# Kernel tuning notes

Hardware: AMD Instinct MI355X
Metric: run time of the kernel (lower is better)

Reference implementation:

```python
import jax, jax.numpy as jnp
import numpy as np

H, I, E, K = 1024, 2816, 8, 2  # hidden, intermediate, n_experts, topk
B, S = 2, 2048


def setup_inputs() -> dict:
    key = jax.random.key(0)
    ks = jax.random.split(key, 6)
    def init(k, shape, fan_in):
        return (jax.random.normal(k, shape, jnp.float32) / np.sqrt(fan_in)).astype(jnp.float32)
    return {
        "x": jax.random.normal(ks[0], (B, S, H), jnp.float32),
        "Wgate": init(ks[1], (H, E), H),   # gating Linear weight (in,out layout)
        "bgate": jnp.zeros((E,), jnp.float32),  # gating Linear bias (nn.Linear default bias=True)
        "Wg": init(ks[2], (E, H, I), H),   # stacked gate_proj, mlp_bias=False
        "Wu": init(ks[3], (E, H, I), H),   # stacked up_proj
        "Wd": init(ks[4], (E, I, H), I),   # stacked down_proj
    }


def reference(x, Wgate, bgate, Wg, Wu, Wd):
    Bb, Ss, Hd = x.shape
    xf = x.reshape(-1, Hd)                       # [N, H] flattened tokens
    logits = xf @ Wgate + bgate                  # [N, E] gate logits
    topv, topi = jax.lax.top_k(logits, K)        # [N, K]
    N = xf.shape[0]
    # sparse combine weights: raw top-k LOGITS (no softmax), zeros elsewhere
    # (faithful to torch: scatter of logits_topk into -inf mask; -inf slots
    #  are never read since only selected experts contribute)
    combine = jnp.zeros_like(logits).at[jnp.arange(N)[:, None], topi].set(topv)  # [N, E]
    # dense grouped SwiGLU over all experts, then sparse combine
    g = jnp.einsum('nh,ehi->nei', xf, Wg)        # [N, E, I]
    u = jnp.einsum('nh,ehi->nei', xf, Wu)        # [N, E, I]
    h = jax.nn.silu(g) * u                       # [N, E, I]
    eo = jnp.einsum('nei,eih->neh', h, Wd)       # [N, E, H]
    out = jnp.einsum('neh,ne->nh', eo, combine).reshape(Bb, Ss, Hd)
    return out, logits
```

## Files before the change

### kernel.cpp

```cpp
#include <hip/hip_runtime.h>

#define HDIM 1024
#define IDIM 2816
#define NEXP 8
#define NTOK 4096
#define NROWS 8192
#define RPAD 8320
#define MAXT 71
#define GU_NYT 44
#define DN_NYT 8
#define GU_NWG (MAXT * GU_NYT)
#define DN_NWG (MAXT * DN_NYT)

typedef short bf16x8 __attribute__((ext_vector_type(8)));
typedef float f32x4 __attribute__((ext_vector_type(4)));
typedef unsigned short u16x8 __attribute__((ext_vector_type(8)));

static __device__ __forceinline__ unsigned short f2bf(float f) {
    union { float f; unsigned int i; } v; v.f = f;
    return (unsigned short)((v.i + 0x7fffu + ((v.i >> 16) & 1u)) >> 16);
}

static __device__ __forceinline__ void gload16(const void* g, void* l) {
    __builtin_amdgcn_global_load_lds(
        (const __attribute__((address_space(1))) unsigned int*)g,
        (__attribute__((address_space(3))) unsigned int*)l, 16, 0, 0);
}

__global__ __launch_bounds__(256) void gating_kernel(
    const float* __restrict__ x, const float* __restrict__ Wgate,
    const float* __restrict__ bgate, float* __restrict__ logits_out,
    int* __restrict__ counts, int* __restrict__ topi, float* __restrict__ topv)
{
    int wave = (blockIdx.x << 2) + (threadIdx.x >> 6);
    int lane = threadIdx.x & 63;
    if (wave >= NTOK) return;
    const float* xr = x + (size_t)wave * HDIM;

    double acc[NEXP];
#pragma unroll
    for (int e = 0; e < NEXP; ++e) acc[e] = 0.0;

    for (int it = 0; it < HDIM / 64; ++it) {
        int h = lane + (it << 6);
        float xv = xr[h];
        const float* wr = Wgate + (size_t)h * NEXP;
#pragma unroll
        for (int e = 0; e < NEXP; ++e) acc[e] += (double)xv * (double)wr[e];
    }
#pragma unroll
    for (int e = 0; e < NEXP; ++e) {
        double v = acc[e];
        for (int off = 32; off; off >>= 1) v += __shfl_xor(v, off, 64);
        acc[e] = v + (double)bgate[e];
    }
    float lf[NEXP];
#pragma unroll
    for (int e = 0; e < NEXP; ++e) lf[e] = (float)acc[e];

    if (lane < NEXP) logits_out[(size_t)wave * NEXP + lane] = lf[lane];

    if (lane == 0) {
        int i1 = 0; float v1 = lf[0];
#pragma unroll
        for (int e = 1; e < NEXP; ++e) if (lf[e] > v1) { v1 = lf[e]; i1 = e; }
        int i2 = -1; float v2 = -3.0e38f;
#pragma unroll
        for (int e = 0; e < NEXP; ++e) {
            if (e == i1) continue;
            if (lf[e] > v2) { v2 = lf[e]; i2 = e; }
        }
        topi[wave * 2 + 0] = i1; topv[wave * 2 + 0] = v1;
        topi[wave * 2 + 1] = i2; topv[wave * 2 + 1] = v2;
        atomicAdd(&counts[i1], 1);
        atomicAdd(&counts[i2], 1);
    }
}

__global__ void offsets_kernel(const int* __restrict__ counts,
                               int* __restrict__ offs, int* __restrict__ cursor,
                               int* __restrict__ ntile, int* __restrict__ te,
                               int* __restrict__ tm0)
{
    if (threadIdx.x == 0 && blockIdx.x == 0) {
        int s = 0;
        for (int e = 0; e < NEXP; ++e) { offs[e] = s; cursor[e] = s; s += counts[e]; }
        offs[NEXP] = s;
        int nt = 0;
        for (int e = 0; e < NEXP; ++e) {
            int c = counts[e], base = offs[e];
            for (int mt = 0; mt * 128 < c; ++mt) { te[nt] = e; tm0[nt] = base + mt * 128; ++nt; }
        }
        *ntile = nt;
    }
}

__global__ __launch_bounds__(256) void scatter_kernel(
    const float* __restrict__ x, const int* __restrict__ topi,
    const float* __restrict__ topv, int* __restrict__ cursor,
    float* __restrict__ row_w, int* __restrict__ tok_of,
    unsigned short* __restrict__ Xg)
{
    int p = (blockIdx.x << 2) + (threadIdx.x >> 6);
    int lane = threadIdx.x & 63;
    if (p >= NROWS) return;
    int n = p >> 1;
    int e = topi[p];
    float w = topv[p];
    int pos = 0;
    if (lane == 0) {
        pos = atomicAdd(&cursor[e], 1);
        row_w[pos] = w;
        tok_of[pos] = n;
    }
    pos = __shfl(pos, 0, 64);
    const float* xr = x + (size_t)n * HDIM;
    unsigned short* dst = Xg + (size_t)pos * HDIM;
#pragma unroll
    for (int it = 0; it < HDIM / 256; ++it) {
        int idx = (it * 64 + lane) * 4;
        float4 v = *reinterpret_cast<const float4*>(&xr[idx]);
        ushort4 o;
        o.x = f2bf(v.x); o.y = f2bf(v.y); o.z = f2bf(v.z); o.w = f2bf(v.w);
        *reinterpret_cast<ushort4*>(&dst[idx]) = o;
    }
}

__global__ __launch_bounds__(256) void transpose_cvt_gu_kernel(
    const float* __restrict__ Wg, const float* __restrict__ Wu,
    unsigned short* __restrict__ W2)
{
    __shared__ unsigned short lds[64 * 66];
    const int kind = blockIdx.z;
    const int e = blockIdx.y;
    const float* s0 = (kind ? Wu : Wg) + (size_t)e * HDIM * IDIM;
    unsigned short* d0 = W2 + (size_t)e * 2 * IDIM * HDIM;
    const int TC = IDIM / 64;
    int tt = blockIdx.x;
    int tr = tt / TC, tc = tt % TC;
    int tid = threadIdx.x;
    {
        int r = tid >> 2, c0 = (tid & 3) << 4;
        const float* s = s0 + (size_t)(tr * 64 + r) * IDIM + tc * 64 + c0;
        float4 v0 = *reinterpret_cast<const float4*>(s);
        float4 v1 = *reinterpret_cast<const float4*>(s + 4);
        float4 v2 = *reinterpret_cast<const float4*>(s + 8);
        float4 v3 = *reinterpret_cast<const float4*>(s + 12);
        unsigned short* lr_ = &lds[r * 66 + c0];
        lr_[0]  = f2bf(v0.x); lr_[1]  = f2bf(v0.y); lr_[2]  = f2bf(v0.z); lr_[3]  = f2bf(v0.w);
        lr_[4]  = f2bf(v1.x); lr_[5]  = f2bf(v1.y); lr_[6]  = f2bf(v1.z); lr_[7]  = f2bf(v1.w);
        lr_[8]  = f2bf(v2.x); lr_[9]  = f2bf(v2.y); lr_[10] = f2bf(v2.z); lr_[11] = f2bf(v2.w);
        lr_[12] = f2bf(v3.x); lr_[13] = f2bf(v3.y); lr_[14] = f2bf(v3.z); lr_[15] = f2bf(v3.w);
    }
    __syncthreads();
    {
        int c = tid >> 2, q0 = (tid & 3) << 4;
        u16x8 o0, o1;
#pragma unroll
        for (int j = 0; j < 8; ++j) o0[j] = lds[(q0 + j) * 66 + c];
#pragma unroll
        for (int j = 0; j < 8; ++j) o1[j] = lds[(q0 + 8 + j) * 66 + c];
        int i = tc * 64 + c;
        int r2 = ((i >> 4) << 5) + (kind << 4) + (i & 15);
        unsigned short* d = d0 + (size_t)r2 * HDIM + tr * 64 + q0;
        *reinterpret_cast<u16x8*>(d) = o0;
        *reinterpret_cast<u16x8*>(d + 8) = o1;
    }
}

__global__ __launch_bounds__(256) void transpose_cvt_d_kernel(
    const float* __restrict__ Wd, unsigned short* __restrict__ Wdt)
{
    __shared__ unsigned short lds[64 * 66];
    const int e = blockIdx.y;
    const float* s0 = Wd + (size_t)e * IDIM * HDIM;
    unsigned short* d0 = Wdt + (size_t)e * HDIM * IDIM;
    const int TC = HDIM / 64;
    int tt = blockIdx.x;
    int tr = tt / TC, tc = tt % TC;
    int tid = threadIdx.x;
    {
        int r = tid >> 2, c0 = (tid & 3) << 4;
        const float* s = s0 + (size_t)(tr * 64 + r) * HDIM + tc * 64 + c0;
        float4 v0 = *reinterpret_cast<const float4*>(s);
        float4 v1 = *reinterpret_cast<const float4*>(s + 4);
        float4 v2 = *reinterpret_cast<const float4*>(s + 8);
        float4 v3 = *reinterpret_cast<const float4*>(s + 12);
        unsigned short* lr_ = &lds[r * 66 + c0];
        lr_[0]  = f2bf(v0.x); lr_[1]  = f2bf(v0.y); lr_[2]  = f2bf(v0.z); lr_[3]  = f2bf(v0.w);
        lr_[4]  = f2bf(v1.x); lr_[5]  = f2bf(v1.y); lr_[6]  = f2bf(v1.z); lr_[7]  = f2bf(v1.w);
        lr_[8]  = f2bf(v2.x); lr_[9]  = f2bf(v2.y); lr_[10] = f2bf(v2.z); lr_[11] = f2bf(v2.w);
        lr_[12] = f2bf(v3.x); lr_[13] = f2bf(v3.y); lr_[14] = f2bf(v3.z); lr_[15] = f2bf(v3.w);
    }
    __syncthreads();
    {
        int c = tid >> 2, q0 = (tid & 3) << 4;
        u16x8 o0, o1;
#pragma unroll
        for (int j = 0; j < 8; ++j) o0[j] = lds[(q0 + j) * 66 + c];
#pragma unroll
        for (int j = 0; j < 8; ++j) o1[j] = lds[(q0 + 8 + j) * 66 + c];
        unsigned short* d = d0 + (size_t)(tc * 64 + c) * IDIM + tr * 64 + q0;
        *reinterpret_cast<u16x8*>(d) = o0;
        *reinterpret_cast<u16x8*>(d + 8) = o1;
    }
}

__global__ __launch_bounds__(256, 4) void gateup_kernel(
    const unsigned short* __restrict__ Xg,
    const unsigned short* __restrict__ W2,
    const int* __restrict__ offs,
    const int* __restrict__ ntile, const int* __restrict__ te,
    const int* __restrict__ tm0, unsigned short* __restrict__ hbuf)
{
    __shared__ unsigned short As[128 * 64];
    __shared__ unsigned short Bs[128 * 64];

    int bid = blockIdx.x;
    int xcd = bid & 7, rest = bid >> 3;
    const int q = GU_NWG / 8, r = GU_NWG % 8;
    int wg = (xcd < r ? xcd * (q + 1) : r * (q + 1) + (xcd - r) * q) + rest;
    int t = wg % MAXT;
    int ny = wg / MAXT;

    if (t >= *ntile) return;
    const int e = te[t];
    const int m0 = tm0[t];
    const int r1 = offs[e + 1];
    const int n0 = ny * 128;

    const unsigned short* wb = W2 + (size_t)e * 2 * IDIM * HDIM;

    const int tid = threadIdx.x;
    const int lane = tid & 63, wv = tid >> 6;
    const int wr = (wv >> 1) * 64, wc = (wv & 1) * 64;
    const int lr = lane & 15, kg = (lane >> 4) * 8;
    const int srow = lane >> 3;
    const int scol = (lane & 7) * 8;

    f32x4 zero = {0.f, 0.f, 0.f, 0.f};
    f32x4 acc[4][4];
#pragma unroll
    for (int m = 0; m < 4; ++m)
#pragma unroll
        for (int n = 0; n < 4; ++n) acc[m][n] = zero;

    for (int k0 = 0; k0 < HDIM; k0 += 64) {
        __syncthreads();
#pragma unroll
        for (int i = 0; i < 4; ++i) {
            int chunk = i * 4 + wv;
            int row = chunk * 8 + srow;
            gload16(&Xg[(size_t)(m0 + row) * HDIM + k0 + scol], &As[chunk * 512 + lane * 8]);
            gload16(&wb[(size_t)(n0 + row) * HDIM + k0 + scol], &Bs[chunk * 512 + lane * 8]);
        }
        __syncthreads();

#pragma unroll
        for (int ks = 0; ks < 2; ++ks) {
            bf16x8 af[4], bf[4];
#pragma unroll
            for (int m = 0; m < 4; ++m)
                af[m] = *reinterpret_cast<const bf16x8*>(&As[(wr + m * 16 + lr) * 64 + ks * 32 + kg]);
#pragma unroll
            for (int n = 0; n < 4; ++n)
                bf[n] = *reinterpret_cast<const bf16x8*>(&Bs[(wc + n * 16 + lr) * 64 + ks * 32 + kg]);
#pragma unroll
            for (int m = 0; m < 4; ++m)
#pragma unroll
                for (int n = 0; n < 4; ++n)
                    acc[m][n] = __builtin_amdgcn_mfma_f32_16x16x32_bf16(af[m], bf[n], acc[m][n], 0, 0, 0);
        }
    }

    const int rr = (lane >> 4) * 4;
    const int iloc0 = ((wc >> 5) << 4) + lr;
    const int col0 = ny * 64 + iloc0;
#pragma unroll
    for (int m = 0; m < 4; ++m) {
#pragma unroll
        for (int j = 0; j < 4; ++j) {
            int grow = m0 + wr + m * 16 + rr + j;
            if (grow < r1) {
                unsigned short* hr = &hbuf[(size_t)grow * IDIM + col0];
                float g0 = acc[m][0][j], u0 = acc[m][1][j];
                float g1 = acc[m][2][j], u1 = acc[m][3][j];
                hr[0]  = f2bf(g0 / (1.0f + __expf(-g0)) * u0);
                hr[16] = f2bf(g1 / (1.0f + __expf(-g1)) * u1);
            }
        }
    }
}

__global__ __launch_bounds__(256, 4) void down_kernel(
    const unsigned short* __restrict__ hbuf,
    const unsigned short* __restrict__ Wdt,
    const int* __restrict__ offs,
    const int* __restrict__ ntile, const int* __restrict__ te,
    const int* __restrict__ tm0,
    const float* __restrict__ row_w, const int* __restrict__ tok_of,
    float* __restrict__ out)
{
    __shared__ unsigned short As[128 * 64];
    __shared__ unsigned short Bs[128 * 64];

    int bid = blockIdx.x;
    int xcd = bid & 7, rest = bid >> 3;
    int wg = xcd * (DN_NWG / 8) + rest;
    int t = wg % MAXT;
    int ny = wg / MAXT;

    if (t >= *ntile) return;
    const int e = te[t];
    const int m0 = tm0[t];
    const int r1 = offs[e + 1];
    const int n0 = ny * 128;

    const unsigned short* wd = Wdt + (size_t)e * HDIM * IDIM;

    const int tid = threadIdx.x;
    const int lane = tid & 63, wv = tid >> 6;
    const int wr = (wv >> 1) * 64, wc = (wv & 1) * 64;
    const int lr = lane & 15, kg = (lane >> 4) * 8;
    const int srow = lane >> 3;
    const int scol = (lane & 7) * 8;

    f32x4 zero = {0.f, 0.f, 0.f, 0.f};
    f32x4 acc[4][4];
#pragma unroll
    for (int m = 0; m < 4; ++m)
#pragma unroll
        for (int n = 0; n < 4; ++n) acc[m][n] = zero;

    for (int k0 = 0; k0 < IDIM; k0 += 64) {
        __syncthreads();
#pragma unroll
        for (int i = 0; i < 4; ++i) {
            int chunk = i * 4 + wv;
            int row = chunk * 8 + srow;
            gload16(&hbuf[(size_t)(m0 + row) * IDIM + k0 + scol], &As[chunk * 512 + lane * 8]);
            gload16(&wd[(size_t)(n0 + row) * IDIM + k0 + scol], &Bs[chunk * 512 + lane * 8]);
        }
        __syncthreads();

#pragma unroll
        for (int ks = 0; ks < 2; ++ks) {
            bf16x8 af[4], bf[4];
#pragma unroll
            for (int m = 0; m < 4; ++m)
                af[m] = *reinterpret_cast<const bf16x8*>(&As[(wr + m * 16 + lr) * 64 + ks * 32 + kg]);
#pragma unroll
            for (int n = 0; n < 4; ++n)
                bf[n] = *reinterpret_cast<const bf16x8*>(&Bs[(wc + n * 16 + lr) * 64 + ks * 32 + kg]);
#pragma unroll
            for (int m = 0; m < 4; ++m)
#pragma unroll
                for (int n = 0; n < 4; ++n)
                    acc[m][n] = __builtin_amdgcn_mfma_f32_16x16x32_bf16(af[m], bf[n], acc[m][n], 0, 0, 0);
        }
    }

    const int rr = (lane >> 4) * 4;
#pragma unroll
    for (int m = 0; m < 4; ++m) {
#pragma unroll
        for (int j = 0; j < 4; ++j) {
            int grow = m0 + wr + m * 16 + rr + j;
            if (grow < r1) {
                float w = row_w[grow];
                int tok = tok_of[grow];
                float* orow = out + (size_t)tok * HDIM + n0 + wc + lr;
#pragma unroll
                for (int n = 0; n < 4; ++n)
                    atomicAdd(&orow[n * 16], acc[m][n][j] * w);
            }
        }
    }
}

extern "C" void kernel_launch(void* const* d_in, const int* in_sizes, int n_in,
                              void* d_out, int out_size, void* d_ws, size_t ws_size,
                              hipStream_t stream)
{
    const float* x     = (const float*)d_in[0];
    const float* Wgate = (const float*)d_in[1];
    const float* bgate = (const float*)d_in[2];
    const float* Wg    = (const float*)d_in[3];
    const float* Wu    = (const float*)d_in[4];
    const float* Wd    = (const float*)d_in[5];
    float* out = (float*)d_out;
    float* logits = out + (size_t)NTOK * HDIM;

    char* ws = (char*)d_ws;
    unsigned short* Xg   = (unsigned short*)ws;
    unsigned short* hbuf = (unsigned short*)(ws + 17039360);
    unsigned short* W2   = (unsigned short*)(ws + 63897600);
    char* meta = ws + 156172288;
    int*   counts = (int*)(meta);
    int*   offs   = (int*)(meta + 64);
    int*   cursor = (int*)(meta + 128);
    int*   ntile  = (int*)(meta + 192);
    int*   te     = (int*)(meta + 256);
    int*   tm0    = (int*)(meta + 768);
    int*   topi   = (int*)(meta + 2048);
    float* topv   = (float*)(meta + 34816);
    float* row_w  = (float*)(meta + 67584);
    int*   tok_of = (int*)(meta + 100352);

    hipMemsetAsync(counts, 0, 32, stream);
    hipMemsetAsync(out, 0, (size_t)NTOK * HDIM * sizeof(float), stream);

    gating_kernel<<<NTOK / 4, 256, 0, stream>>>(x, Wgate, bgate, logits, counts, topi, topv);
    offsets_kernel<<<1, 64, 0, stream>>>(counts, offs, cursor, ntile, te, tm0);
    scatter_kernel<<<NROWS / 4, 256, 0, stream>>>(x, topi, topv, cursor, row_w, tok_of, Xg);

    transpose_cvt_gu_kernel<<<dim3((HDIM / 64) * (IDIM / 64), NEXP, 2), 256, 0, stream>>>(Wg, Wu, W2);

    gateup_kernel<<<GU_NWG, 256, 0, stream>>>(Xg, W2, offs, ntile, te, tm0, hbuf);

    transpose_cvt_d_kernel<<<dim3((IDIM / 64) * (HDIM / 64), NEXP), 256, 0, stream>>>(Wd, W2);

    down_kernel<<<DN_NWG, 256, 0, stream>>>(hbuf, W2, offs, ntile, te, tm0, row_w, tok_of, out);
}
```

Before: 515.2 us.

## Fuse weight transpose and bf16 conversion into grouped GEMM B-tile loads

Removes the two separate transpose/convert kernels for gate/up and down weights. The GEMM kernels now read fp32 weights directly, convert them to bf16 in registers and write them into LDS in a transposed, XOR-swizzled layout. The A loads are swizzled to match. The gate-up grid is regrouped so that 8 consecutive M-tiles share the same N-slice, for better weight reuse in L2. This avoids writing and rereading roughly 140MB of bf16 weights. In exchange, each tile reloads fp32 weights with scalar, non-async loads, and the conversion is now repeated in every workgroup that touches the same weight tile.

Measured after the change: 668.8 us. 1.3x slower.

```diff
diff --git a/kernel.cpp b/kernel.cpp
--- a/kernel.cpp
+++ b/kernel.cpp
@@ -9,12 +9,13 @@
 #define MAXT 71
 #define GU_NYT 44
 #define DN_NYT 8
-#define GU_NWG (MAXT * GU_NYT)
+#define GU_TG 8
+#define GU_NTG 9
+#define GU_NWG (GU_NTG * GU_NYT * GU_TG)
 #define DN_NWG (MAXT * DN_NYT)
 
 typedef short bf16x8 __attribute__((ext_vector_type(8)));
 typedef float f32x4 __attribute__((ext_vector_type(4)));
-typedef unsigned short u16x8 __attribute__((ext_vector_type(8)));
 
 static __device__ __forceinline__ unsigned short f2bf(float f) {
     union { float f; unsigned int i; } v; v.f = f;
@@ -126,89 +127,9 @@
     }
 }
 
-__global__ __launch_bounds__(256) void transpose_cvt_gu_kernel(
-    const float* __restrict__ Wg, const float* __restrict__ Wu,
-    unsigned short* __restrict__ W2)
-{
-    __shared__ unsigned short lds[64 * 66];
-    const int kind = blockIdx.z;
-    const int e = blockIdx.y;
-    const float* s0 = (kind ? Wu : Wg) + (size_t)e * HDIM * IDIM;
-    unsigned short* d0 = W2 + (size_t)e * 2 * IDIM * HDIM;
-    const int TC = IDIM / 64;
-    int tt = blockIdx.x;
-    int tr = tt / TC, tc = tt % TC;
-    int tid = threadIdx.x;
-    {
-        int r = tid >> 2, c0 = (tid & 3) << 4;
-        const float* s = s0 + (size_t)(tr * 64 + r) * IDIM + tc * 64 + c0;
-        float4 v0 = *reinterpret_cast<const float4*>(s);
-        float4 v1 = *reinterpret_cast<const float4*>(s + 4);
-        float4 v2 = *reinterpret_cast<const float4*>(s + 8);
-        float4 v3 = *reinterpret_cast<const float4*>(s + 12);
-        unsigned short* lr_ = &lds[r * 66 + c0];
-        lr_[0]  = f2bf(v0.x); lr_[1]  = f2bf(v0.y); lr_[2]  = f2bf(v0.z); lr_[3]  = f2bf(v0.w);
-        lr_[4]  = f2bf(v1.x); lr_[5]  = f2bf(v1.y); lr_[6]  = f2bf(v1.z); lr_[7]  = f2bf(v1.w);
-        lr_[8]  = f2bf(v2.x); lr_[9]  = f2bf(v2.y); lr_[10] = f2bf(v2.z); lr_[11] = f2bf(v2.w);
-        lr_[12] = f2bf(v3.x); lr_[13] = f2bf(v3.y); lr_[14] = f2bf(v3.z); lr_[15] = f2bf(v3.w);
-    }
-    __syncthreads();
-    {
-        int c = tid >> 2, q0 = (tid & 3) << 4;
-        u16x8 o0, o1;
-#pragma unroll
-        for (int j = 0; j < 8; ++j) o0[j] = lds[(q0 + j) * 66 + c];
-#pragma unroll
-        for (int j = 0; j < 8; ++j) o1[j] = lds[(q0 + 8 + j) * 66 + c];
-        int i = tc * 64 + c;
-        int r2 = ((i >> 4) << 5) + (kind << 4) + (i & 15);
-        unsigned short* d = d0 + (size_t)r2 * HDIM + tr * 64 + q0;
-        *reinterpret_cast<u16x8*>(d) = o0;
-        *reinterpret_cast<u16x8*>(d + 8) = o1;
-    }
-}
-
-__global__ __launch_bounds__(256) void transpose_cvt_d_kernel(
-    const float* __restrict__ Wd, unsigned short* __restrict__ Wdt)
-{
-    __shared__ unsigned short lds[64 * 66];
-    const int e = blockIdx.y;
-    const float* s0 = Wd + (size_t)e * IDIM * HDIM;
-    unsigned short* d0 = Wdt + (size_t)e * HDIM * IDIM;
-    const int TC = HDIM / 64;
-    int tt = blockIdx.x;
-    int tr = tt / TC, tc = tt % TC;
-    int tid = threadIdx.x;
-    {
-        int r = tid >> 2, c0 = (tid & 3) << 4;
-        const float* s = s0 + (size_t)(tr * 64 + r) * HDIM + tc * 64 + c0;
-        float4 v0 = *reinterpret_cast<const float4*>(s);
-        float4 v1 = *reinterpret_cast<const float4*>(s + 4);
-        float4 v2 = *reinterpret_cast<const float4*>(s + 8);
-        float4 v3 = *reinterpret_cast<const float4*>(s + 12);
-        unsigned short* lr_ = &lds[r * 66 + c0];
-        lr_[0]  = f2bf(v0.x); lr_[1]  = f2bf(v0.y); lr_[2]  = f2bf(v0.z); lr_[3]  = f2bf(v0.w);
-        lr_[4]  = f2bf(v1.x); lr_[5]  = f2bf(v1.y); lr_[6]  = f2bf(v1.z); lr_[7]  = f2bf(v1.w);
-        lr_[8]  = f2bf(v2.x); lr_[9]  = f2bf(v2.y); lr_[10] = f2bf(v2.z); lr_[11] = f2bf(v2.w);
-        lr_[12] = f2bf(v3.x); lr_[13] = f2bf(v3.y); lr_[14] = f2bf(v3.z); lr_[15] = f2bf(v3.w);
-    }
-    __syncthreads();
-    {
-        int c = tid >> 2, q0 = (tid & 3) << 4;
-        u16x8 o0, o1;
-#pragma unroll
-        for (int j = 0; j < 8; ++j) o0[j] = lds[(q0 + j) * 66 + c];
-#pragma unroll
-        for (int j = 0; j < 8; ++j) o1[j] = lds[(q0 + 8 + j) * 66 + c];
-        unsigned short* d = d0 + (size_t)(tc * 64 + c) * IDIM + tr * 64 + q0;
-        *reinterpret_cast<u16x8*>(d) = o0;
-        *reinterpret_cast<u16x8*>(d + 8) = o1;
-    }
-}
-
 __global__ __launch_bounds__(256, 4) void gateup_kernel(
     const unsigned short* __restrict__ Xg,
-    const unsigned short* __restrict__ W2,
+    const float* __restrict__ Wg, const float* __restrict__ Wu,
     const int* __restrict__ offs,
     const int* __restrict__ ntile, const int* __restrict__ te,
     const int* __restrict__ tm0, unsigned short* __restrict__ hbuf)
@@ -218,25 +139,34 @@
 
     int bid = blockIdx.x;
     int xcd = bid & 7, rest = bid >> 3;
-    const int q = GU_NWG / 8, r = GU_NWG % 8;
-    int wg = (xcd < r ? xcd * (q + 1) : r * (q + 1) + (xcd - r) * q) + rest;
-    int t = wg % MAXT;
-    int ny = wg / MAXT;
-
+    int wg = xcd * (GU_NWG / 8) + rest;
+    int tg = wg / (GU_NYT * GU_TG);
+    int r2 = wg % (GU_NYT * GU_TG);
+    int ny = r2 >> 3, ti = r2 & 7;
+    int t = tg * GU_TG + ti;
     if (t >= *ntile) return;
+
     const int e = te[t];
     const int m0 = tm0[t];
     const int r1 = offs[e + 1];
-    const int n0 = ny * 128;
-
-    const unsigned short* wb = W2 + (size_t)e * 2 * IDIM * HDIM;
+    const int n0i = ny * 64;
+
+    const float* wgp = Wg + (size_t)e * HDIM * IDIM;
+    const float* wup = Wu + (size_t)e * HDIM * IDIM;
 
     const int tid = threadIdx.x;
     const int lane = tid & 63, wv = tid >> 6;
     const int wr = (wv >> 1) * 64, wc = (wv & 1) * 64;
-    const int lr = lane & 15, kg = (lane >> 4) * 8;
-    const int srow = lane >> 3;
-    const int scol = (lane & 7) * 8;
+    const int lr = lane & 15, kq16 = lane >> 4;
+
+    const int a_row8 = tid >> 3;
+    const int a_c16 = tid & 7;
+    const int bn = tid & 127;
+    const int bsrc = (bn >> 4) & 1;
+    const int biloc = ((bn >> 5) << 4) | (bn & 15);
+    const float* bbase = (bsrc ? wup : wgp) + n0i + biloc;
+    const int kq_hi = tid >> 7;
+    const int bswz_row = bn * 64;
 
     f32x4 zero = {0.f, 0.f, 0.f, 0.f};
     f32x4 acc[4][4];
@@ -247,12 +177,30 @@
 
     for (int k0 = 0; k0 < HDIM; k0 += 64) {
         __syncthreads();
-#pragma unroll
-        for (int i = 0; i < 4; ++i) {
-            int chunk = i * 4 + wv;
-            int row = chunk * 8 + srow;
-            gload16(&Xg[(size_t)(m0 + row) * HDIM + k0 + scol], &As[chunk * 512 + lane * 8]);
-            gload16(&wb[(size_t)(n0 + row) * HDIM + k0 + scol], &Bs[chunk * 512 + lane * 8]);
+        unsigned int bpack[8][2];
+#pragma unroll
+        for (int u = 0; u < 8; ++u) {
+            int kq = u * 2 + kq_hi;
+            const float* sp = bbase + (size_t)(k0 + kq * 4) * IDIM;
+            float v0 = sp[0];
+            float v1 = sp[IDIM];
+            float v2 = sp[2 * IDIM];
+            float v3 = sp[3 * IDIM];
+            bpack[u][0] = (unsigned)f2bf(v0) | ((unsigned)f2bf(v1) << 16);
+            bpack[u][1] = (unsigned)f2bf(v2) | ((unsigned)f2bf(v3) << 16);
+        }
+#pragma unroll
+        for (int ch = 0; ch < 4; ++ch) {
+            int row = ch * 32 + a_row8;
+            int c16s = a_c16 ^ (row & 7);
+            gload16(&Xg[(size_t)(m0 + row) * HDIM + k0 + c16s * 8],
+                    &As[ch * 2048 + tid * 8]);
+        }
+#pragma unroll
+        for (int u = 0; u < 8; ++u) {
+            int kq = u * 2 + kq_hi;
+            int soff = bswz_row + (((kq >> 1) ^ (bn & 7)) << 3) + ((kq & 1) << 2);
+            *reinterpret_cast<uint2*>(&Bs[soff]) = *reinterpret_cast<uint2*>(bpack[u]);
         }
         __syncthreads();
 
@@ -260,11 +208,17 @@
         for (int ks = 0; ks < 2; ++ks) {
             bf16x8 af[4], bf[4];
 #pragma unroll
-            for (int m = 0; m < 4; ++m)
-                af[m] = *reinterpret_cast<const bf16x8*>(&As[(wr + m * 16 + lr) * 64 + ks * 32 + kg]);
-#pragma unroll
-            for (int n = 0; n < 4; ++n)
-                bf[n] = *reinterpret_cast<const bf16x8*>(&Bs[(wc + n * 16 + lr) * 64 + ks * 32 + kg]);
+            for (int m = 0; m < 4; ++m) {
+                int row = wr + m * 16 + lr;
+                int sw = (ks * 4 + kq16) ^ (row & 7);
+                af[m] = *reinterpret_cast<const bf16x8*>(&As[row * 64 + sw * 8]);
+            }
+#pragma unroll
+            for (int n = 0; n < 4; ++n) {
+                int row = wc + n * 16 + lr;
+                int sw = (ks * 4 + kq16) ^ (row & 7);
+                bf[n] = *reinterpret_cast<const bf16x8*>(&Bs[row * 64 + sw * 8]);
+            }
 #pragma unroll
             for (int m = 0; m < 4; ++m)
 #pragma unroll
@@ -294,7 +248,7 @@
 
 __global__ __launch_bounds__(256, 4) void down_kernel(
     const unsigned short* __restrict__ hbuf,
-    const unsigned short* __restrict__ Wdt,
+    const float* __restrict__ Wd,
     const int* __restrict__ offs,
     const int* __restrict__ ntile, const int* __restrict__ te,
     const int* __restrict__ tm0,
@@ -309,21 +263,26 @@
     int wg = xcd * (DN_NWG / 8) + rest;
     int t = wg % MAXT;
     int ny = wg / MAXT;
-
     if (t >= *ntile) return;
+
     const int e = te[t];
     const int m0 = tm0[t];
     const int r1 = offs[e + 1];
     const int n0 = ny * 128;
 
-    const unsigned short* wd = Wdt + (size_t)e * HDIM * IDIM;
+    const float* wd = Wd + (size_t)e * IDIM * HDIM;
 
     const int tid = threadIdx.x;
     const int lane = tid & 63, wv = tid >> 6;
     const int wr = (wv >> 1) * 64, wc = (wv & 1) * 64;
-    const int lr = lane & 15, kg = (lane >> 4) * 8;
-    const int srow = lane >> 3;
-    const int scol = (lane & 7) * 8;
+    const int lr = lane & 15, kq16 = lane >> 4;
+
+    const int a_row8 = tid >> 3;
+    const int a_c16 = tid & 7;
+    const int bn = tid & 127;
+    const float* bbase = wd + n0 + bn;
+    const int kq_hi = tid >> 7;
+    const int bswz_row = bn * 64;
 
     f32x4 zero = {0.f, 0.f, 0.f, 0.f};
     f32x4 acc[4][4];
@@ -334,12 +293,30 @@
 
     for (int k0 = 0; k0 < IDIM; k0 += 64) {
         __syncthreads();
-#pragma unroll
-        for (int i = 0; i < 4; ++i) {
-            int chunk = i * 4 + wv;
-            int row = chunk * 8 + srow;
-            gload16(&hbuf[(size_t)(m0 + row) * IDIM + k0 + scol], &As[chunk * 512 + lane * 8]);
-            gload16(&wd[(size_t)(n0 + row) * IDIM + k0 + scol], &Bs[chunk * 512 + lane * 8]);
+        unsigned int bpack[8][2];
+#pragma unroll
+        for (int u = 0; u < 8; ++u) {
+            int kq = u * 2 + kq_hi;
+            const float* sp = bbase + (size_t)(k0 + kq * 4) * HDIM;
+            float v0 = sp[0];
+            float v1 = sp[HDIM];
+            float v2 = sp[2 * HDIM];
+            float v3 = sp[3 * HDIM];
+            bpack[u][0] = (unsigned)f2bf(v0) | ((unsigned)f2bf(v1) << 16);
+            bpack[u][1] = (unsigned)f2bf(v2) | ((unsigned)f2bf(v3) << 16);
+        }
+#pragma unroll
+        for (int ch = 0; ch < 4; ++ch) {
+            int row = ch * 32 + a_row8;
+            int c16s = a_c16 ^ (row & 7);
+            gload16(&hbuf[(size_t)(m0 + row) * IDIM + k0 + c16s * 8],
+                    &As[ch * 2048 + tid * 8]);
+        }
+#pragma unroll
+        for (int u = 0; u < 8; ++u) {
+            int kq = u * 2 + kq_hi;
+            int soff = bswz_row + (((kq >> 1) ^ (bn & 7)) << 3) + ((kq & 1) << 2);
+            *reinterpret_cast<uint2*>(&Bs[soff]) = *reinterpret_cast<uint2*>(bpack[u]);
         }
         __syncthreads();
 
@@ -347,11 +324,17 @@
         for (int ks = 0; ks < 2; ++ks) {
             bf16x8 af[4], bf[4];
 #pragma unroll
-            for (int m = 0; m < 4; ++m)
-                af[m] = *reinterpret_cast<const bf16x8*>(&As[(wr + m * 16 + lr) * 64 + ks * 32 + kg]);
-#pragma unroll
-            for (int n = 0; n < 4; ++n)
-                bf[n] = *reinterpret_cast<const bf16x8*>(&Bs[(wc + n * 16 + lr) * 64 + ks * 32 + kg]);
+            for (int m = 0; m < 4; ++m) {
+                int row = wr + m * 16 + lr;
+                int sw = (ks * 4 + kq16) ^ (row & 7);
+                af[m] = *reinterpret_cast<const bf16x8*>(&As[row * 64 + sw * 8]);
+            }
+#pragma unroll
+            for (int n = 0; n < 4; ++n) {
+                int row = wc + n * 16 + lr;
+                int sw = (ks * 4 + kq16) ^ (row & 7);
+                bf[n] = *reinterpret_cast<const bf16x8*>(&Bs[row * 64 + sw * 8]);
+            }
 #pragma unroll
             for (int m = 0; m < 4; ++m)
 #pragma unroll
@@ -394,8 +377,7 @@
     char* ws = (char*)d_ws;
     unsigned short* Xg   = (unsigned short*)ws;
     unsigned short* hbuf = (unsigned short*)(ws + 17039360);
-    unsigned short* W2   = (unsigned short*)(ws + 63897600);
-    char* meta = ws + 156172288;
+    char* meta = ws + 63897600;
     int*   counts = (int*)(meta);
     int*   offs   = (int*)(meta + 64);
     int*   cursor = (int*)(meta + 128);
@@ -414,11 +396,6 @@
     offsets_kernel<<<1, 64, 0, stream>>>(counts, offs, cursor, ntile, te, tm0);
     scatter_kernel<<<NROWS / 4, 256, 0, stream>>>(x, topi, topv, cursor, row_w, tok_of, Xg);
 
-    transpose_cvt_gu_kernel<<<dim3((HDIM / 64) * (IDIM / 64), NEXP, 2), 256, 0, stream>>>(Wg, Wu, W2);
-
-    gateup_kernel<<<GU_NWG, 256, 0, stream>>>(Xg, W2, offs, ntile, te, tm0, hbuf);
-
-    transpose_cvt_d_kernel<<<dim3((IDIM / 64) * (HDIM / 64), NEXP), 256, 0, stream>>>(Wd, W2);
-
-    down_kernel<<<DN_NWG, 256, 0, stream>>>(hbuf, W2, offs, ntile, te, tm0, row_w, tok_of, out);
-}
+    gateup_kernel<<<GU_NWG, 256, 0, stream>>>(Xg, Wg, Wu, offs, ntile, te, tm0, hbuf);
+    down_kernel<<<DN_NWG, 256, 0, stream>>>(hbuf, Wd, offs, ntile, te, tm0, row_w, tok_of, out);
+}
```

## Swizzle LDS tiles with XOR and regroup workgroup tile order for L2 reuse

Applied to the files above, without the earlier changes.

Loads A and B tiles into shared memory with an XOR swizzle of 16-byte column groups by row, and applies the matching swizzle on the MFMA fragment reads. This targets LDS bank conflicts from the row-stride-64 layout. It also remaps workgroup IDs so groups of 8 M-tiles share each N-tile (gate/up) and consecutive tiles share an XCD (down), aiming for better weight and activation reuse in L2. GU_NWG grows to 9*44*8, which adds some early-exit blocks.

New measurement: 483.3 us. 1.07x faster.

```diff
diff --git a/kernel.cpp b/kernel.cpp
--- a/kernel.cpp
+++ b/kernel.cpp
@@ -9,7 +9,9 @@
 #define MAXT 71
 #define GU_NYT 44
 #define DN_NYT 8
-#define GU_NWG (MAXT * GU_NYT)
+#define GU_TG 8
+#define GU_NTG 9
+#define GU_NWG (GU_NTG * GU_NYT * GU_TG)
 #define DN_NWG (MAXT * DN_NYT)
 
 typedef short bf16x8 __attribute__((ext_vector_type(8)));
@@ -218,12 +220,13 @@
 
     int bid = blockIdx.x;
     int xcd = bid & 7, rest = bid >> 3;
-    const int q = GU_NWG / 8, r = GU_NWG % 8;
-    int wg = (xcd < r ? xcd * (q + 1) : r * (q + 1) + (xcd - r) * q) + rest;
-    int t = wg % MAXT;
-    int ny = wg / MAXT;
-
+    int wg = xcd * (GU_NWG / 8) + rest;
+    int tg = wg / (GU_NYT * GU_TG);
+    int r2 = wg % (GU_NYT * GU_TG);
+    int ny = r2 >> 3, ti = r2 & 7;
+    int t = tg * GU_TG + ti;
     if (t >= *ntile) return;
+
     const int e = te[t];
     const int m0 = tm0[t];
     const int r1 = offs[e + 1];
@@ -234,9 +237,10 @@
     const int tid = threadIdx.x;
     const int lane = tid & 63, wv = tid >> 6;
     const int wr = (wv >> 1) * 64, wc = (wv & 1) * 64;
-    const int lr = lane & 15, kg = (lane >> 4) * 8;
-    const int srow = lane >> 3;
-    const int scol = (lane & 7) * 8;
+    const int lr = lane & 15, kq16 = lane >> 4;
+
+    const int a_row8 = tid >> 3;
+    const int a_c16 = tid & 7;
 
     f32x4 zero = {0.f, 0.f, 0.f, 0.f};
     f32x4 acc[4][4];
@@ -248,11 +252,11 @@
     for (int k0 = 0; k0 < HDIM; k0 += 64) {
         __syncthreads();
 #pragma unroll
-        for (int i = 0; i < 4; ++i) {
-            int chunk = i * 4 + wv;
-            int row = chunk * 8 + srow;
-            gload16(&Xg[(size_t)(m0 + row) * HDIM + k0 + scol], &As[chunk * 512 + lane * 8]);
-            gload16(&wb[(size_t)(n0 + row) * HDIM + k0 + scol], &Bs[chunk * 512 + lane * 8]);
+        for (int ch = 0; ch < 4; ++ch) {
+            int row = ch * 32 + a_row8;
+            int c16s = a_c16 ^ (row & 7);
+            gload16(&Xg[(size_t)(m0 + row) * HDIM + k0 + c16s * 8], &As[ch * 2048 + tid * 8]);
+            gload16(&wb[(size_t)(n0 + row) * HDIM + k0 + c16s * 8], &Bs[ch * 2048 + tid * 8]);
         }
         __syncthreads();
 
@@ -260,11 +264,17 @@
         for (int ks = 0; ks < 2; ++ks) {
             bf16x8 af[4], bf[4];
 #pragma unroll
-            for (int m = 0; m < 4; ++m)
-                af[m] = *reinterpret_cast<const bf16x8*>(&As[(wr + m * 16 + lr) * 64 + ks * 32 + kg]);
-#pragma unroll
-            for (int n = 0; n < 4; ++n)
-                bf[n] = *reinterpret_cast<const bf16x8*>(&Bs[(wc + n * 16 + lr) * 64 + ks * 32 + kg]);
+            for (int m = 0; m < 4; ++m) {
+                int row = wr + m * 16 + lr;
+                int sw = (ks * 4 + kq16) ^ (row & 7);
+                af[m] = *reinterpret_cast<const bf16x8*>(&As[row * 64 + sw * 8]);
+            }
+#pragma unroll
+            for (int n = 0; n < 4; ++n) {
+                int row = wc + n * 16 + lr;
+                int sw = (ks * 4 + kq16) ^ (row & 7);
+                bf[n] = *reinterpret_cast<const bf16x8*>(&Bs[row * 64 + sw * 8]);
+            }
 #pragma unroll
             for (int m = 0; m < 4; ++m)
 #pragma unroll
@@ -307,10 +317,10 @@
     int bid = blockIdx.x;
     int xcd = bid & 7, rest = bid >> 3;
     int wg = xcd * (DN_NWG / 8) + rest;
-    int t = wg % MAXT;
-    int ny = wg / MAXT;
-
+    int t = wg >> 3;
+    int ny = wg & 7;
     if (t >= *ntile) return;
+
     const int e = te[t];
     const int m0 = tm0[t];
     const int r1 = offs[e + 1];
@@ -321,9 +331,10 @@
     const int tid = threadIdx.x;
     const int lane = tid & 63, wv = tid >> 6;
     const int wr = (wv >> 1) * 64, wc = (wv & 1) * 64;
-    const int lr = lane & 15, kg = (lane >> 4) * 8;
-    const int srow = lane >> 3;
-    const int scol = (lane & 7) * 8;
+    const int lr = lane & 15, kq16 = lane >> 4;
+
+    const int a_row8 = tid >> 3;
+    const int a_c16 = tid & 7;
 
     f32x4 zero = {0.f, 0.f, 0.f, 0.f};
     f32x4 acc[4][4];
@@ -335,11 +346,11 @@
     for (int k0 = 0; k0 < IDIM; k0 += 64) {
         __syncthreads();
 #pragma unroll
-        for (int i = 0; i < 4; ++i) {
-            int chunk = i * 4 + wv;
-            int row = chunk * 8 + srow;
-            gload16(&hbuf[(size_t)(m0 + row) * IDIM + k0 + scol], &As[chunk * 512 + lane * 8]);
-            gload16(&wd[(size_t)(n0 + row) * IDIM + k0 + scol], &Bs[chunk * 512 + lane * 8]);
+        for (int ch = 0; ch < 4; ++ch) {
+            int row = ch * 32 + a_row8;
+            int c16s = a_c16 ^ (row & 7);
+            gload16(&hbuf[(size_t)(m0 + row) * IDIM + k0 + c16s * 8], &As[ch * 2048 + tid * 8]);
+            gload16(&wd[(size_t)(n0 + row) * IDIM + k0 + c16s * 8], &Bs[ch * 2048 + tid * 8]);
         }
         __syncthreads();
 
@@ -347,11 +358,17 @@
         for (int ks = 0; ks < 2; ++ks) {
             bf16x8 af[4], bf[4];
 #pragma unroll
-            for (int m = 0; m < 4; ++m)
-                af[m] = *reinterpret_cast<const bf16x8*>(&As[(wr + m * 16 + lr) * 64 + ks * 32 + kg]);
-#pragma unroll
-            for (int n = 0; n < 4; ++n)
-                bf[n] = *reinterpret_cast<const bf16x8*>(&Bs[(wc + n * 16 + lr) * 64 + ks * 32 + kg]);
+            for (int m = 0; m < 4; ++m) {
+                int row = wr + m * 16 + lr;
+                int sw = (ks * 4 + kq16) ^ (row & 7);
+                af[m] = *reinterpret_cast<const bf16x8*>(&As[row * 64 + sw * 8]);
+            }
+#pragma unroll
+            for (int n = 0; n < 4; ++n) {
+                int row = wc + n * 16 + lr;
+                int sw = (ks * 4 + kq16) ^ (row & 7);
+                bf[n] = *reinterpret_cast<const bf16x8*>(&Bs[row * 64 + sw * 8]);
+            }
 #pragma unroll
             for (int m = 0; m < 4; ++m)
 #pragma unroll
```
